# Kernel optimization log

Measured on AMD Instinct MI355X. Metric: run time of the kernel, lower is better.

The kernel has to match this reference:

```python
import jax, jax.numpy as jnp
import numpy as np

VOCAB, D_IN, D_H, N_REL, N_CLS = 10000, 256, 256, 3, 4
N_NODES, N_EDGES, N_GRAPHS = 100000, 300000, 512


def setup_inputs() -> dict:
    key = jax.random.key(0)
    ks = jax.random.split(key, 12)
    x = jax.random.randint(ks[0], (N_NODES,), 0, VOCAB)
    edge_index = jax.random.randint(ks[1], (2, N_EDGES), 0, N_NODES)
    edge_type = jax.random.randint(ks[2], (N_EDGES,), 0, N_REL)
    batch = jnp.sort(jax.random.randint(ks[3], (N_NODES,), 0, N_GRAPHS))
    s = 0.05
    embed_table = jax.random.normal(ks[4], (VOCAB, D_IN), jnp.float32) * s
    embed_table = embed_table.at[0].set(0.0)  # padding_idx=0
    W1 = jax.random.normal(ks[5], (N_REL, D_IN, D_H), jnp.float32) * s
    root1 = jax.random.normal(ks[6], (D_IN, D_H), jnp.float32) * s
    b1 = jnp.zeros((D_H,), jnp.float32)
    W2 = jax.random.normal(ks[7], (N_REL, D_H, D_H), jnp.float32) * s
    root2 = jax.random.normal(ks[8], (D_H, D_H), jnp.float32) * s
    b2 = jnp.zeros((D_H,), jnp.float32)
    lin_W = jax.random.normal(ks[9], (D_H, N_CLS), jnp.float32) * s
    lin_b = jnp.zeros((N_CLS,), jnp.float32)
    return {"x": x, "edge_index": edge_index, "edge_type": edge_type,
            "batch": batch, "num_graphs": N_GRAPHS,
            "embed_table": embed_table, "W1": W1, "root1": root1, "b1": b1,
            "W2": W2, "root2": root2, "b2": b2, "lin_W": lin_W, "lin_b": lin_b}


def rgcn_conv(h, W, root, b, src, dst, edge_type, n_nodes):
    # PyG RGCNConv: out = h @ root + b + sum_r mean_{edges of rel r into i}(h[src] @ W_r)
    out = h @ root + b
    for r in range(W.shape[0]):
        hr = h @ W[r]                                   # [N, d_out] dense GEMM
        mask = (edge_type == r)
        msg = jnp.where(mask[:, None], hr[src], 0.0)    # [E, d_out]
        agg = jax.ops.segment_sum(msg, dst, num_segments=n_nodes)
        cnt = jax.ops.segment_sum(mask.astype(h.dtype), dst, num_segments=n_nodes)
        out = out + agg / jnp.maximum(cnt, 1.0)[:, None]
    return out


def reference(x, edge_index, edge_type, batch, num_graphs,
              embed_table, W1, root1, b1, W2, root2, b2, lin_W, lin_b):
    n_nodes = x.shape[0]
    src, dst = edge_index[0], edge_index[1]
    h = embed_table[x]                                  # [N, D_IN]
    h = jax.nn.relu(rgcn_conv(h, W1, root1, b1, src, dst, edge_type, n_nodes))
    h = jax.nn.relu(rgcn_conv(h, W2, root2, b2, src, dst, edge_type, n_nodes))
    # global mean pool by graph id
    sums = jax.ops.segment_sum(h, batch, num_segments=num_graphs)
    cnts = jax.ops.segment_sum(jnp.ones((n_nodes,), h.dtype), batch, num_segments=num_graphs)
    g = sums / jnp.maximum(cnts, 1.0)[:, None]          # [G, D_H]
    return g @ lin_W + lin_b                            # [G, N_CLS]
```

## Files before the change

### kernel.cpp

```cpp
#include <hip/hip_runtime.h>

#define D 256
#define SB 1024
typedef __attribute__((ext_vector_type(8))) short short8;
typedef __attribute__((ext_vector_type(4))) float floatx4;

__device__ __forceinline__ unsigned short f2bf(float f) {
  unsigned int u = __float_as_uint(f);
  u = (u + 0x7FFF + ((u >> 16) & 1)) >> 16;
  return (unsigned short)u;
}
__device__ __forceinline__ float bf2f(unsigned short h) {
  return __uint_as_float(((unsigned int)h) << 16);
}

__device__ __forceinline__ void glds16(const void* g, void* l) {
  __builtin_amdgcn_global_load_lds(
      (const __attribute__((address_space(1))) unsigned int*)g,
      (__attribute__((address_space(3))) unsigned int*)l, 16, 0, 0);
}

__global__ __launch_bounds__(256) void k_setup(
    int* __restrict__ cur, int RN,
    const int* __restrict__ batch, int* __restrict__ gstart, int N, int G,
    const float* __restrict__ table, unsigned short* __restrict__ tableb, int TN,
    const float* __restrict__ root1, const float* __restrict__ W1,
    const float* __restrict__ root2, const float* __restrict__ W2,
    unsigned short* __restrict__ wb, int* __restrict__ zrowi,
    int g0, int g1, int g2, int g3) {
  int b = blockIdx.x, t = threadIdx.x;
  if (b < g0) {
    int i = b * 1024 + t * 4;
#pragma unroll
    for (int j = 0; j < 4; j++) if (i + j < RN) cur[i + j] = 0;
    if (b == 0 && t < 128) zrowi[t] = 0;
  } else if (b < g1) {
    int i = (b - g0) * 256 + t;
    if (i >= N) return;
    int bb = batch[i];
    if (i == 0) { for (int g = 0; g <= bb; g++) gstart[g] = 0; }
    else { int pb = batch[i - 1]; for (int g = pb + 1; g <= bb; g++) gstart[g] = i; }
    if (i == N - 1) { for (int g = bb + 1; g <= G; g++) gstart[g] = N; }
  } else if (b < g2) {
    int i = (b - g1) * 256 + t;
    if (i < TN) tableb[i] = f2bf(table[i]);
  } else {
    int layer = (b < g3) ? 0 : 1;
    int idx = ((b - (layer ? g3 : g2)) * 256 + t);
    int mat = idx >> 16, rem = idx & 65535;
    int n = rem >> 8, k = rem & 255;
    const float* root = layer ? root2 : root1;
    const float* W = layer ? W2 : W1;
    const float* s = (mat == 0) ? root : (W + (size_t)(mat - 1) * 65536);
    wb[(size_t)layer * 4 * 65536 + idx] = f2bf(s[k * 256 + n]);
  }
}

__global__ __launch_bounds__(256) void k_count_i(const int* __restrict__ dst,
    const int* __restrict__ et, int* __restrict__ cnt, int E, int N) {
  int e = blockIdx.x * 256 + threadIdx.x;
  if (e >= E) return;
  atomicAdd(&cnt[et[e] * N + dst[e]], 1);
}

__global__ __launch_bounds__(256) void k_scan1(const int* __restrict__ in,
    int* __restrict__ bsum, int n) {
  __shared__ int s[256];
  int base = blockIdx.x * SB, t = threadIdx.x;
  int a = 0;
#pragma unroll
  for (int j = 0; j < 4; j++) { int i = base + t * 4 + j; if (i < n) a += in[i]; }
  s[t] = a; __syncthreads();
  for (int o = 128; o > 0; o >>= 1) { if (t < o) s[t] += s[t + o]; __syncthreads(); }
  if (t == 0) bsum[blockIdx.x] = s[0];
}

__global__ __launch_bounds__(256) void k_scan2(int* __restrict__ bsum, int nb,
    int* __restrict__ total_out) {
  __shared__ int s[256];
  int t = threadIdx.x;
  int v[4]; int a = 0;
#pragma unroll
  for (int j = 0; j < 4; j++) {
    int i = t * 4 + j;
    v[j] = (i < nb) ? bsum[i] : 0;
    a += v[j];
  }
  s[t] = a; __syncthreads();
  for (int o = 1; o < 256; o <<= 1) {
    int x_ = (t >= o) ? s[t - o] : 0;
    __syncthreads();
    s[t] += x_;
    __syncthreads();
  }
  int excl = (t > 0) ? s[t - 1] : 0;
#pragma unroll
  for (int j = 0; j < 4; j++) {
    int i = t * 4 + j;
    if (i < nb) { bsum[i] = excl; excl += v[j]; }
  }
  if (t == 255) *total_out = s[255];
}

__global__ __launch_bounds__(256) void k_scan3(const int* __restrict__ in,
    const int* __restrict__ bsum, int* __restrict__ off, int* __restrict__ cur,
    int n) {
  __shared__ int s[256];
  int base = blockIdx.x * SB, t = threadIdx.x;
  int v[4]; int a = 0;
#pragma unroll
  for (int j = 0; j < 4; j++) {
    int i = base + t * 4 + j;
    v[j] = (i < n) ? in[i] : 0;
    a += v[j];
  }
  s[t] = a; __syncthreads();
  for (int o = 1; o < 256; o <<= 1) {
    int x_ = (t >= o) ? s[t - o] : 0;
    __syncthreads();
    s[t] += x_;
    __syncthreads();
  }
  int excl = (t > 0 ? s[t - 1] : 0) + bsum[blockIdx.x];
#pragma unroll
  for (int j = 0; j < 4; j++) {
    int i = base + t * 4 + j;
    if (i < n) { off[i] = excl; cur[i] = excl; excl += v[j]; }
  }
}

__global__ __launch_bounds__(256) void k_place2(const int* __restrict__ src,
    const int* __restrict__ dst, const int* __restrict__ et,
    const int* __restrict__ x, int* __restrict__ cur,
    int* __restrict__ esx, int* __restrict__ ess, int E, int N) {
  int e = blockIdx.x * 256 + threadIdx.x;
  if (e >= E) return;
  int s = src[e];
  int pos = atomicAdd(&cur[et[e] * N + dst[e]], 1);
  esx[pos] = x[s];
  ess[pos] = s;
}

__global__ __launch_bounds__(256) void k_agg(const unsigned short* __restrict__ h,
    const int* __restrict__ rows, const int* __restrict__ off,
    unsigned short* __restrict__ out, int RN) {
  const int wave = threadIdx.x >> 6, lane = threadIdx.x & 63;
  const int base = (blockIdx.x * 4 + wave) * 8;
  if (base >= RN) return;

  int lo[8], hi[8];
#pragma unroll
  for (int j = 0; j < 8; j++) {
    int id = base + j;
    lo[j] = (id < RN) ? off[id] : 0;
    hi[j] = (id < RN) ? off[id + 1] : 0;
    if (hi[j] - lo[j] < 2) hi[j] = lo[j];
  }

  int r0[8];
#pragma unroll
  for (int j = 0; j < 8; j++)
    r0[j] = (hi[j] > lo[j]) ? rows[lo[j]] : 0;

  ushort4 v0[8];
#pragma unroll
  for (int j = 0; j < 8; j++)
    v0[j] = (hi[j] > lo[j])
        ? *(const ushort4*)(h + (size_t)r0[j] * D + lane * 4)
        : make_ushort4(0, 0, 0, 0);

  float a[8][4];
#pragma unroll
  for (int j = 0; j < 8; j++) {
    a[j][0] = bf2f(v0[j].x); a[j][1] = bf2f(v0[j].y);
    a[j][2] = bf2f(v0[j].z); a[j][3] = bf2f(v0[j].w);
  }

#pragma unroll
  for (int j = 0; j < 8; j++) {
    for (int p = lo[j] + 1; p < hi[j]; ++p) {
      int r = rows[p];
      ushort4 v = *(const ushort4*)(h + (size_t)r * D + lane * 4);
      a[j][0] += bf2f(v.x); a[j][1] += bf2f(v.y);
      a[j][2] += bf2f(v.z); a[j][3] += bf2f(v.w);
    }
  }

#pragma unroll
  for (int j = 0; j < 8; j++) {
    int id = base + j;
    if (id >= RN) continue;
    int c = hi[j] - lo[j];
    if (c < 2) continue;
    float inv = 1.0f / (float)c;
    ushort4 o;
    o.x = f2bf(a[j][0] * inv); o.y = f2bf(a[j][1] * inv);
    o.z = f2bf(a[j][2] * inv); o.w = f2bf(a[j][3] * inv);
    *(ushort4*)(out + (size_t)id * D + lane * 4) = o;
  }
}

__global__ __launch_bounds__(512) void k_lgemm(
    const unsigned short* __restrict__ Aroot, const int* __restrict__ gidx,
    const unsigned short* agg, const int* __restrict__ rows_,
    const int* __restrict__ off_, const unsigned short* __restrict__ zrow,
    const unsigned short* __restrict__ wb,
    const float* __restrict__ bias, unsigned short* Cout, int M, int N) {
  __shared__ unsigned short AsU[2][128 * 32];
  __shared__ unsigned short BsU[2][256 * 32];
  const int tid = threadIdx.x;
  const int w = tid >> 6, lane = tid & 63;
  const int wr = w >> 2, wc = w & 3;
  const int i0 = blockIdx.x * 128;
  const int ml = lane & 15, q = lane >> 4;

  const int arow = w * 16 + (lane >> 2);
  const int achunk = lane & 3;
  int ra = i0 + arow;
  int rac = (ra < M) ? ra : (M - 1);
  const int rowA0 = gidx ? gidx[rac] : rac;
  const unsigned short* abase[4];
  abase[0] = Aroot + (size_t)rowA0 * D + achunk * 8;
#pragma unroll
  for (int r = 0; r < 3; r++) {
    int id = r * N + rac;
    int lo = off_[id];
    int cnt = off_[id + 1] - lo;
    const unsigned short* b;
    if (cnt == 0) b = zrow;
    else if (cnt == 1) b = Aroot + (size_t)rows_[lo] * D;
    else b = agg + (size_t)id * D;
    abase[r + 1] = b + achunk * 8;
  }

  const int brow = w * 32 + (lane >> 2);
  const int bchunk = lane & 3;
  const size_t bofs = (size_t)brow * D + bchunk * 8;

  floatx4 acc[4][4];
#pragma unroll
  for (int i = 0; i < 4; i++)
#pragma unroll
    for (int j = 0; j < 4; j++) acc[i][j] = (floatx4){0.f, 0.f, 0.f, 0.f};

  unsigned short* aldst[2] = {&AsU[0][w * 512], &AsU[1][w * 512]};
  unsigned short* bldst0[2] = {&BsU[0][w * 1024], &BsU[1][w * 1024]};
  unsigned short* bldst1[2] = {&BsU[0][w * 1024 + 512], &BsU[1][w * 1024 + 512]};

  for (int step = 0; step < 16; ++step) {
    __syncthreads();
#pragma unroll
    for (int h = 0; h < 2; h++) {
      const int kabs = step * 64 + h * 32;
      const int seg = kabs >> 8, kloc = kabs & 255;
      glds16(abase[seg] + kloc, aldst[h]);
      const unsigned short* bb = wb + (size_t)seg * 65536 + bofs + kloc;
      glds16(bb, bldst0[h]);
      glds16(bb + 16 * D, bldst1[h]);
    }
    __syncthreads();

#pragma unroll
    for (int h = 0; h < 2; h++) {
      short8 aF[4], bF[4];
#pragma unroll
      for (int mi = 0; mi < 4; mi++)
        aF[mi] = *(const short8*)&AsU[h][(wr * 64 + mi * 16 + ml) * 32 + q * 8];
#pragma unroll
      for (int ni = 0; ni < 4; ni++)
        bF[ni] = *(const short8*)&BsU[h][(wc * 64 + ni * 16 + ml) * 32 + q * 8];
#pragma unroll
      for (int mi = 0; mi < 4; mi++)
#pragma unroll
        for (int ni = 0; ni < 4; ni++)
          acc[mi][ni] = __builtin_amdgcn_mfma_f32_16x16x32_bf16(
              aF[mi], bF[ni], acc[mi][ni], 0, 0, 0);
    }
  }

  __syncthreads();

  float bv[4];
#pragma unroll
  for (int ni = 0; ni < 4; ni++) bv[ni] = bias[wc * 64 + ni * 16 + ml];
#pragma unroll
  for (int mi = 0; mi < 4; mi++) {
#pragma unroll
    for (int ni = 0; ni < 4; ni++) {
      int col = wc * 64 + ni * 16 + ml;
#pragma unroll
      for (int j = 0; j < 4; j++) {
        int row = i0 + wr * 64 + mi * 16 + q * 4 + j;
        if (row < M) {
          float v = fmaxf(acc[mi][ni][j] + bv[ni], 0.f);
          Cout[(size_t)row * D + col] = f2bf(v);
        }
      }
    }
  }
}

__global__ __launch_bounds__(256) void k_poolfinal(
    const unsigned short* __restrict__ h, const int* __restrict__ gstart,
    const float* __restrict__ linW, const float* __restrict__ linb,
    float* __restrict__ out, int G) {
  __shared__ float red[4][D];
  __shared__ float sred[4][4];
  int g = blockIdx.x;
  int lo = gstart[g], hi = gstart[g + 1];
  int tid = threadIdx.x, wave = tid >> 6, lane = tid & 63;
  float a0 = 0.f, a1 = 0.f, a2 = 0.f, a3 = 0.f;
  for (int i = lo + wave; i < hi; i += 4) {
    ushort4 v = *(const ushort4*)(h + (size_t)i * D + lane * 4);
    a0 += bf2f(v.x); a1 += bf2f(v.y); a2 += bf2f(v.z); a3 += bf2f(v.w);
  }
  red[wave][lane * 4 + 0] = a0;
  red[wave][lane * 4 + 1] = a1;
  red[wave][lane * 4 + 2] = a2;
  red[wave][lane * 4 + 3] = a3;
  __syncthreads();
  float s = red[0][tid] + red[1][tid] + red[2][tid] + red[3][tid];
  float inv = (hi > lo) ? 1.0f / (float)(hi - lo) : 0.0f;
  float m = s * inv;
  float4 wrow = *(const float4*)(linW + tid * 4);
  float p0 = m * wrow.x, p1 = m * wrow.y, p2 = m * wrow.z, p3 = m * wrow.w;
  for (int o = 32; o > 0; o >>= 1) {
    p0 += __shfl_down(p0, o, 64);
    p1 += __shfl_down(p1, o, 64);
    p2 += __shfl_down(p2, o, 64);
    p3 += __shfl_down(p3, o, 64);
  }
  if (lane == 0) {
    sred[wave][0] = p0; sred[wave][1] = p1;
    sred[wave][2] = p2; sred[wave][3] = p3;
  }
  __syncthreads();
  if (tid < 4)
    out[g * 4 + tid] = sred[0][tid] + sred[1][tid] + sred[2][tid] +
                       sred[3][tid] + linb[tid];
}

extern "C" void kernel_launch(void* const* d_in, const int* in_sizes, int n_in,
                              void* d_out, int out_size, void* d_ws, size_t ws_size,
                              hipStream_t stream) {
  const int*   x     = (const int*)d_in[0];
  const int*   ei    = (const int*)d_in[1];
  const int*   et    = (const int*)d_in[2];
  const int*   batch = (const int*)d_in[3];
  const float* table = (const float*)d_in[5];
  const float* W1    = (const float*)d_in[6];
  const float* root1 = (const float*)d_in[7];
  const float* b1    = (const float*)d_in[8];
  const float* W2    = (const float*)d_in[9];
  const float* root2 = (const float*)d_in[10];
  const float* b2    = (const float*)d_in[11];
  const float* linW  = (const float*)d_in[12];
  const float* linb  = (const float*)d_in[13];
  float* out = (float*)d_out;

  const int N = in_sizes[0];
  const int E = in_sizes[2];
  const int G = out_size / 4;
  const int VOC = in_sizes[5] / D;
  const int* src = ei;
  const int* dst = ei + E;
  const int RN = 3 * N;

  char* wsb = (char*)d_ws;
  size_t pg = (size_t)N * D * 2;
  unsigned short* P0 = (unsigned short*)wsb;
  unsigned short* P1 = (unsigned short*)(wsb + pg);
  unsigned short* P3 = (unsigned short*)(wsb + 3 * pg);
  unsigned short* wb = (unsigned short*)(wsb + 4 * pg);
  unsigned short* zrow = wb + 2 * 4 * 65536;
  int*   off    = (int*)(zrow + 256);
  int*   esx    = off + (RN + 1);
  int*   ess    = esx + E;
  int*   gstart = ess + E;
  unsigned short* tableb = P3;
  int* cur  = (int*)P0;
  int* bsum = cur + RN;

  const int nb = (RN + SB - 1) / SB;

  int nbZero = (RN + 1023) / 1024;
  int nbBounds = (N + 255) / 256;
  int nbCvt = (VOC * D + 255) / 256;
  int g0 = nbZero, g1 = g0 + nbBounds, g2 = g1 + nbCvt, g3 = g2 + 1024;
  k_setup<<<g3 + 1024, 256, 0, stream>>>(cur, RN, batch, gstart, N, G,
      table, tableb, VOC * D, root1, W1, root2, W2, wb, (int*)zrow,
      g0, g1, g2, g3);

  k_count_i<<<(E + 255) / 256, 256, 0, stream>>>(dst, et, cur, E, N);
  k_scan1<<<nb, 256, 0, stream>>>(cur, bsum, RN);
  k_scan2<<<1, 256, 0, stream>>>(bsum, nb, off + RN);
  k_scan3<<<nb, 256, 0, stream>>>(cur, bsum, off, cur, RN);
  k_place2<<<(E + 255) / 256, 256, 0, stream>>>(src, dst, et, x, cur, esx, ess, E, N);

  const int gagg = (RN + 31) / 32;
  const int ggemm = (N + 127) / 128;

  k_agg<<<gagg, 256, 0, stream>>>(tableb, esx, off, P0, RN);
  k_lgemm<<<ggemm, 512, 0, stream>>>(tableb, x, P0, esx, off, zrow, wb, b1, P0, N, N);
  k_agg<<<gagg, 256, 0, stream>>>(P0, ess, off, P1, RN);
  k_lgemm<<<ggemm, 512, 0, stream>>>(P0, nullptr, P1, ess, off, zrow,
                                     wb + 4 * 65536, b2, P1, N, N);

  k_poolfinal<<<G, 256, 0, stream>>>(P1, gstart, linW, linb, out, G);
}
```

Baseline: 380.7 us.

## Fuse per-relation mean aggregation into GEMM kernel prologue

Removes the standalone aggregation kernel and has each GEMM block compute the mean-aggregated neighbour rows for its own 128 nodes across all three relations before the tiled GEMM starts. The results are still written to the global agg buffer and read back after a vmcnt wait and block barrier, but this saves one launch per layer and keeps the re-read close in time, so it is likely to hit in cache. In exchange the gather runs inside large 512-thread GEMM blocks with only 4 rows in flight per wave. That may cut memory-level parallelism and delay the start of the MFMA main loop.

```diff
diff --git a/kernel.cpp b/kernel.cpp
--- a/kernel.cpp
+++ b/kernel.cpp
@@ -141,68 +141,9 @@
   ess[pos] = s;
 }
 
-__global__ __launch_bounds__(256) void k_agg(const unsigned short* __restrict__ h,
-    const int* __restrict__ rows, const int* __restrict__ off,
-    unsigned short* __restrict__ out, int RN) {
-  const int wave = threadIdx.x >> 6, lane = threadIdx.x & 63;
-  const int base = (blockIdx.x * 4 + wave) * 8;
-  if (base >= RN) return;
-
-  int lo[8], hi[8];
-#pragma unroll
-  for (int j = 0; j < 8; j++) {
-    int id = base + j;
-    lo[j] = (id < RN) ? off[id] : 0;
-    hi[j] = (id < RN) ? off[id + 1] : 0;
-    if (hi[j] - lo[j] < 2) hi[j] = lo[j];
-  }
-
-  int r0[8];
-#pragma unroll
-  for (int j = 0; j < 8; j++)
-    r0[j] = (hi[j] > lo[j]) ? rows[lo[j]] : 0;
-
-  ushort4 v0[8];
-#pragma unroll
-  for (int j = 0; j < 8; j++)
-    v0[j] = (hi[j] > lo[j])
-        ? *(const ushort4*)(h + (size_t)r0[j] * D + lane * 4)
-        : make_ushort4(0, 0, 0, 0);
-
-  float a[8][4];
-#pragma unroll
-  for (int j = 0; j < 8; j++) {
-    a[j][0] = bf2f(v0[j].x); a[j][1] = bf2f(v0[j].y);
-    a[j][2] = bf2f(v0[j].z); a[j][3] = bf2f(v0[j].w);
-  }
-
-#pragma unroll
-  for (int j = 0; j < 8; j++) {
-    for (int p = lo[j] + 1; p < hi[j]; ++p) {
-      int r = rows[p];
-      ushort4 v = *(const ushort4*)(h + (size_t)r * D + lane * 4);
-      a[j][0] += bf2f(v.x); a[j][1] += bf2f(v.y);
-      a[j][2] += bf2f(v.z); a[j][3] += bf2f(v.w);
-    }
-  }
-
-#pragma unroll
-  for (int j = 0; j < 8; j++) {
-    int id = base + j;
-    if (id >= RN) continue;
-    int c = hi[j] - lo[j];
-    if (c < 2) continue;
-    float inv = 1.0f / (float)c;
-    ushort4 o;
-    o.x = f2bf(a[j][0] * inv); o.y = f2bf(a[j][1] * inv);
-    o.z = f2bf(a[j][2] * inv); o.w = f2bf(a[j][3] * inv);
-    *(ushort4*)(out + (size_t)id * D + lane * 4) = o;
-  }
-}
-
 __global__ __launch_bounds__(512) void k_lgemm(
     const unsigned short* __restrict__ Aroot, const int* __restrict__ gidx,
-    const unsigned short* agg, const int* __restrict__ rows_,
+    unsigned short* __restrict__ agg, const int* __restrict__ rows_,
     const int* __restrict__ off_, const unsigned short* __restrict__ zrow,
     const unsigned short* __restrict__ wb,
     const float* __restrict__ bias, unsigned short* Cout, int M, int N) {
@@ -213,6 +154,55 @@
   const int wr = w >> 2, wc = w & 3;
   const int i0 = blockIdx.x * 128;
   const int ml = lane & 15, q = lane >> 4;
+
+  for (int kb = 0; kb < 12; ++kb) {
+    int los[4], his[4], idv[4];
+#pragma unroll
+    for (int j = 0; j < 4; j++) {
+      int m = (kb * 4 + j) * 8 + w;
+      int rel = m >> 7, row = m & 127;
+      int r = i0 + row;
+      int rc = (r < M) ? r : (M - 1);
+      int id = rel * N + rc;
+      int lo = off_[id];
+      int hi = off_[id + 1];
+      idv[j] = id; los[j] = lo;
+      his[j] = (hi - lo >= 2) ? hi : lo;
+    }
+    ushort4 v0[4];
+#pragma unroll
+    for (int j = 0; j < 4; j++)
+      v0[j] = (his[j] > los[j])
+          ? *(const ushort4*)(Aroot + (size_t)rows_[los[j]] * D + lane * 4)
+          : make_ushort4(0, 0, 0, 0);
+    float a4[4][4];
+#pragma unroll
+    for (int j = 0; j < 4; j++) {
+      a4[j][0] = bf2f(v0[j].x); a4[j][1] = bf2f(v0[j].y);
+      a4[j][2] = bf2f(v0[j].z); a4[j][3] = bf2f(v0[j].w);
+    }
+#pragma unroll
+    for (int j = 0; j < 4; j++) {
+      for (int p = los[j] + 1; p < his[j]; ++p) {
+        int rid = rows_[p];
+        ushort4 v = *(const ushort4*)(Aroot + (size_t)rid * D + lane * 4);
+        a4[j][0] += bf2f(v.x); a4[j][1] += bf2f(v.y);
+        a4[j][2] += bf2f(v.z); a4[j][3] += bf2f(v.w);
+      }
+    }
+#pragma unroll
+    for (int j = 0; j < 4; j++) {
+      int c = his[j] - los[j];
+      if (c < 2) continue;
+      float inv = 1.0f / (float)c;
+      ushort4 o;
+      o.x = f2bf(a4[j][0] * inv); o.y = f2bf(a4[j][1] * inv);
+      o.z = f2bf(a4[j][2] * inv); o.w = f2bf(a4[j][3] * inv);
+      *(ushort4*)(agg + (size_t)idv[j] * D + lane * 4) = o;
+    }
+  }
+  asm volatile("s_waitcnt vmcnt(0)" ::: "memory");
+  __syncthreads();
 
   const int arow = w * 16 + (lane >> 2);
   const int achunk = lane & 3;
@@ -397,12 +387,9 @@
   k_scan3<<<nb, 256, 0, stream>>>(cur, bsum, off, cur, RN);
   k_place2<<<(E + 255) / 256, 256, 0, stream>>>(src, dst, et, x, cur, esx, ess, E, N);
 
-  const int gagg = (RN + 31) / 32;
   const int ggemm = (N + 127) / 128;
 
-  k_agg<<<gagg, 256, 0, stream>>>(tableb, esx, off, P0, RN);
   k_lgemm<<<ggemm, 512, 0, stream>>>(tableb, x, P0, esx, off, zrow, wb, b1, P0, N, N);
-  k_agg<<<gagg, 256, 0, stream>>>(P0, ess, off, P1, RN);
   k_lgemm<<<ggemm, 512, 0, stream>>>(P0, nullptr, P1, ess, off, zrow,
                                      wb + 4 * 65536, b2, P1, N, N);
 
```

After: 411.1 us. 8.0% more time.

## Fuse global mean pooling into second GEMM epilogue via float atomics

Applied to the files above, without the earlier changes.

The second layer's GEMM epilogue no longer writes the bf16 hidden state. Each output element is atomically added into a per-graph float sum buffer, and a small kernel then divides by node count and applies the final linear layer. This removes the store and re-read of the full second-layer activation and the separate pooling pass. The cost is tens of millions of float atomics concentrated on a few hundred graph rows, and the pooled sum order is no longer deterministic. Separately, the GEMM main loop drops the two-slice LDS buffering in favour of a single 32-wide K slice per barrier, which doubles the number of synchronisation steps.

```diff
diff --git a/kernel.cpp b/kernel.cpp
--- a/kernel.cpp
+++ b/kernel.cpp
@@ -200,14 +200,20 @@
   }
 }
 
+__global__ __launch_bounds__(256) void k_zerog(float* __restrict__ gsum, int n4) {
+  int i = blockIdx.x * 256 + threadIdx.x;
+  if (i < n4) ((float4*)gsum)[i] = make_float4(0.f, 0.f, 0.f, 0.f);
+}
+
 __global__ __launch_bounds__(512) void k_lgemm(
     const unsigned short* __restrict__ Aroot, const int* __restrict__ gidx,
-    const unsigned short* agg, const int* __restrict__ rows_,
+    const unsigned short* __restrict__ agg, const int* __restrict__ rows_,
     const int* __restrict__ off_, const unsigned short* __restrict__ zrow,
     const unsigned short* __restrict__ wb,
-    const float* __restrict__ bias, unsigned short* Cout, int M, int N) {
-  __shared__ unsigned short AsU[2][128 * 32];
-  __shared__ unsigned short BsU[2][256 * 32];
+    const float* __restrict__ bias, unsigned short* __restrict__ Cout,
+    const int* __restrict__ batchv, float* __restrict__ gsum, int M, int N) {
+  __shared__ unsigned short AsU[128 * 32];
+  __shared__ unsigned short BsU[256 * 32];
   const int tid = threadIdx.x;
   const int w = tid >> 6, lane = tid & 63;
   const int wr = w >> 2, wc = w & 3;
@@ -243,39 +249,32 @@
 #pragma unroll
     for (int j = 0; j < 4; j++) acc[i][j] = (floatx4){0.f, 0.f, 0.f, 0.f};
 
-  unsigned short* aldst[2] = {&AsU[0][w * 512], &AsU[1][w * 512]};
-  unsigned short* bldst0[2] = {&BsU[0][w * 1024], &BsU[1][w * 1024]};
-  unsigned short* bldst1[2] = {&BsU[0][w * 1024 + 512], &BsU[1][w * 1024 + 512]};
-
-  for (int step = 0; step < 16; ++step) {
-    __syncthreads();
-#pragma unroll
-    for (int h = 0; h < 2; h++) {
-      const int kabs = step * 64 + h * 32;
-      const int seg = kabs >> 8, kloc = kabs & 255;
-      glds16(abase[seg] + kloc, aldst[h]);
-      const unsigned short* bb = wb + (size_t)seg * 65536 + bofs + kloc;
-      glds16(bb, bldst0[h]);
-      glds16(bb + 16 * D, bldst1[h]);
-    }
-    __syncthreads();
-
-#pragma unroll
-    for (int h = 0; h < 2; h++) {
-      short8 aF[4], bF[4];
-#pragma unroll
-      for (int mi = 0; mi < 4; mi++)
-        aF[mi] = *(const short8*)&AsU[h][(wr * 64 + mi * 16 + ml) * 32 + q * 8];
+  unsigned short* aldst = &AsU[w * 512];
+  unsigned short* bldst0 = &BsU[w * 1024];
+  unsigned short* bldst1 = &BsU[w * 1024 + 512];
+
+  for (int step = 0; step < 32; ++step) {
+    const int seg = step >> 3, kloc = (step & 7) * 32;
+    __syncthreads();
+    glds16(abase[seg] + kloc, aldst);
+    const unsigned short* bb = wb + (size_t)seg * 65536 + bofs + kloc;
+    glds16(bb, bldst0);
+    glds16(bb + 16 * D, bldst1);
+    __syncthreads();
+
+    short8 aF[4], bF[4];
+#pragma unroll
+    for (int mi = 0; mi < 4; mi++)
+      aF[mi] = *(const short8*)&AsU[(wr * 64 + mi * 16 + ml) * 32 + q * 8];
+#pragma unroll
+    for (int ni = 0; ni < 4; ni++)
+      bF[ni] = *(const short8*)&BsU[(wc * 64 + ni * 16 + ml) * 32 + q * 8];
+#pragma unroll
+    for (int mi = 0; mi < 4; mi++)
 #pragma unroll
       for (int ni = 0; ni < 4; ni++)
-        bF[ni] = *(const short8*)&BsU[h][(wc * 64 + ni * 16 + ml) * 32 + q * 8];
-#pragma unroll
-      for (int mi = 0; mi < 4; mi++)
-#pragma unroll
-        for (int ni = 0; ni < 4; ni++)
-          acc[mi][ni] = __builtin_amdgcn_mfma_f32_16x16x32_bf16(
-              aF[mi], bF[ni], acc[mi][ni], 0, 0, 0);
-    }
+        acc[mi][ni] = __builtin_amdgcn_mfma_f32_16x16x32_bf16(
+            aF[mi], bF[ni], acc[mi][ni], 0, 0, 0);
   }
 
   __syncthreads();
@@ -283,47 +282,58 @@
   float bv[4];
 #pragma unroll
   for (int ni = 0; ni < 4; ni++) bv[ni] = bias[wc * 64 + ni * 16 + ml];
-#pragma unroll
-  for (int mi = 0; mi < 4; mi++) {
-#pragma unroll
-    for (int ni = 0; ni < 4; ni++) {
-      int col = wc * 64 + ni * 16 + ml;
+  if (gsum) {
+#pragma unroll
+    for (int mi = 0; mi < 4; mi++) {
 #pragma unroll
       for (int j = 0; j < 4; j++) {
         int row = i0 + wr * 64 + mi * 16 + q * 4 + j;
-        if (row < M) {
+        if (row >= M) continue;
+        int gb = batchv[row];
+#pragma unroll
+        for (int ni = 0; ni < 4; ni++) {
+          int col = wc * 64 + ni * 16 + ml;
           float v = fmaxf(acc[mi][ni][j] + bv[ni], 0.f);
-          Cout[(size_t)row * D + col] = f2bf(v);
+          atomicAdd(&gsum[(size_t)gb * D + col], v);
         }
       }
     }
-  }
-}
-
-__global__ __launch_bounds__(256) void k_poolfinal(
-    const unsigned short* __restrict__ h, const int* __restrict__ gstart,
+  } else {
+#pragma unroll
+    for (int mi = 0; mi < 4; mi++) {
+#pragma unroll
+      for (int ni = 0; ni < 4; ni++) {
+        int col = wc * 64 + ni * 16 + ml;
+#pragma unroll
+        for (int j = 0; j < 4; j++) {
+          int row = i0 + wr * 64 + mi * 16 + q * 4 + j;
+          if (row < M) {
+            float v = fmaxf(acc[mi][ni][j] + bv[ni], 0.f);
+            Cout[(size_t)row * D + col] = f2bf(v);
+          }
+        }
+      }
+    }
+  }
+}
+
+__global__ __launch_bounds__(64) void k_final(
+    const float* __restrict__ gsum, const int* __restrict__ gstart,
     const float* __restrict__ linW, const float* __restrict__ linb,
     float* __restrict__ out, int G) {
-  __shared__ float red[4][D];
-  __shared__ float sred[4][4];
-  int g = blockIdx.x;
-  int lo = gstart[g], hi = gstart[g + 1];
-  int tid = threadIdx.x, wave = tid >> 6, lane = tid & 63;
-  float a0 = 0.f, a1 = 0.f, a2 = 0.f, a3 = 0.f;
-  for (int i = lo + wave; i < hi; i += 4) {
-    ushort4 v = *(const ushort4*)(h + (size_t)i * D + lane * 4);
-    a0 += bf2f(v.x); a1 += bf2f(v.y); a2 += bf2f(v.z); a3 += bf2f(v.w);
-  }
-  red[wave][lane * 4 + 0] = a0;
-  red[wave][lane * 4 + 1] = a1;
-  red[wave][lane * 4 + 2] = a2;
-  red[wave][lane * 4 + 3] = a3;
-  __syncthreads();
-  float s = red[0][tid] + red[1][tid] + red[2][tid] + red[3][tid];
-  float inv = (hi > lo) ? 1.0f / (float)(hi - lo) : 0.0f;
-  float m = s * inv;
-  float4 wrow = *(const float4*)(linW + tid * 4);
-  float p0 = m * wrow.x, p1 = m * wrow.y, p2 = m * wrow.z, p3 = m * wrow.w;
+  int g = blockIdx.x, lane = threadIdx.x;
+  int cnt = gstart[g + 1] - gstart[g];
+  float inv = (cnt > 0) ? 1.0f / (float)cnt : 0.0f;
+  float4 s = *(const float4*)(gsum + (size_t)g * D + lane * 4);
+  float m0 = s.x * inv, m1 = s.y * inv, m2 = s.z * inv, m3 = s.w * inv;
+  float4 w0 = *(const float4*)(linW + (lane * 4 + 0) * 4);
+  float4 w1 = *(const float4*)(linW + (lane * 4 + 1) * 4);
+  float4 w2 = *(const float4*)(linW + (lane * 4 + 2) * 4);
+  float4 w3 = *(const float4*)(linW + (lane * 4 + 3) * 4);
+  float p0 = m0 * w0.x + m1 * w1.x + m2 * w2.x + m3 * w3.x;
+  float p1 = m0 * w0.y + m1 * w1.y + m2 * w2.y + m3 * w3.y;
+  float p2 = m0 * w0.z + m1 * w1.z + m2 * w2.z + m3 * w3.z;
+  float p3 = m0 * w0.w + m1 * w1.w + m2 * w2.w + m3 * w3.w;
   for (int o = 32; o > 0; o >>= 1) {
     p0 += __shfl_down(p0, o, 64);
     p1 += __shfl_down(p1, o, 64);
@@ -331,13 +341,11 @@
     p3 += __shfl_down(p3, o, 64);
   }
   if (lane == 0) {
-    sred[wave][0] = p0; sred[wave][1] = p1;
-    sred[wave][2] = p2; sred[wave][3] = p3;
-  }
-  __syncthreads();
-  if (tid < 4)
-    out[g * 4 + tid] = sred[0][tid] + sred[1][tid] + sred[2][tid] +
-                       sred[3][tid] + linb[tid];
+    out[g * 4 + 0] = p0 + linb[0];
+    out[g * 4 + 1] = p1 + linb[1];
+    out[g * 4 + 2] = p2 + linb[2];
+    out[g * 4 + 3] = p3 + linb[3];
+  }
 }
 
 extern "C" void kernel_launch(void* const* d_in, const int* in_sizes, int n_in,
@@ -380,6 +388,7 @@
   unsigned short* tableb = P3;
   int* cur  = (int*)P0;
   int* bsum = cur + RN;
+  float* gsum = (float*)((((size_t)esx) + 15) & ~(size_t)15);
 
   const int nb = (RN + SB - 1) / SB;
 
@@ -401,10 +410,15 @@
   const int ggemm = (N + 127) / 128;
 
   k_agg<<<gagg, 256, 0, stream>>>(tableb, esx, off, P0, RN);
-  k_lgemm<<<ggemm, 512, 0, stream>>>(tableb, x, P0, esx, off, zrow, wb, b1, P0, N, N);
+  k_lgemm<<<ggemm, 512, 0, stream>>>(tableb, x, P0, esx, off, zrow, wb, b1,
+                                     P0, nullptr, nullptr, N, N);
+
+  k_zerog<<<(G * D / 4 + 255) / 256, 256, 0, stream>>>(gsum, G * D / 4);
+
   k_agg<<<gagg, 256, 0, stream>>>(P0, ess, off, P1, RN);
   k_lgemm<<<ggemm, 512, 0, stream>>>(P0, nullptr, P1, ess, off, zrow,
-                                     wb + 4 * 65536, b2, P1, N, N);
-
-  k_poolfinal<<<G, 256, 0, stream>>>(P1, gstart, linW, linb, out, G);
-}
+                                     wb + 4 * 65536, b2, nullptr, batch, gsum,
+                                     N, N);
+
+  k_final<<<G, 64, 0, stream>>>(gsum, gstart, linW, linb, out, G);
+}
```

Measured after the change: 659.1 us. 1.73x slower.
